# Optimization experiments

Measured on AMD Instinct MI355X. Metric: run time of the kernel, lower is better.

Reference implementation:

```python
import jax, jax.numpy as jnp
import numpy as np

B, N, D, H, ND = 16, 512, 768, 12, 32
DK = D // H  # 64
GRID = 11    # hard-coded 11x11 patch grid in SpatialCirclePosition.patch


def setup_inputs() -> dict:
    key = jax.random.key(0)
    ks = jax.random.split(key, 10)
    features = jax.random.normal(ks[0], (B, N, D), dtype=jnp.float32)
    boxes = jax.random.uniform(ks[1], (B, N, 4), dtype=jnp.float32)  # normalized [0,1]
    sizes_wh = jax.random.randint(ks[2], (B, 2), 512, 1024).astype(jnp.int32)
    image_sizes = jnp.concatenate([sizes_wh, sizes_wh], axis=-1)  # (B,4) = [w,h,w,h]
    s = 0.02
    Wq = jax.random.normal(ks[3], (D, D), dtype=jnp.float32) * s
    Wk = jax.random.normal(ks[4], (D, D), dtype=jnp.float32) * s
    Wv = jax.random.normal(ks[5], (D, D), dtype=jnp.float32) * s
    Wo = jax.random.normal(ks[6], (D, D), dtype=jnp.float32) * s
    bq = jnp.zeros((D,), jnp.float32); bk = jnp.zeros((D,), jnp.float32)
    bv = jnp.zeros((D,), jnp.float32); bo = jnp.zeros((D,), jnp.float32)
    gamma = jnp.ones((D,), jnp.float32); beta = jnp.zeros((D,), jnp.float32)
    dist_emb = jax.random.normal(ks[7], (ND, H), dtype=jnp.float32) * s
    return {"features": features, "boxes": boxes, "image_sizes": image_sizes,
            "Wq": Wq, "bq": bq, "Wk": Wk, "bk": bk, "Wv": Wv, "bv": bv,
            "Wo": Wo, "bo": bo, "gamma": gamma, "beta": beta, "dist_emb": dist_emb}


def _patch_bins(boxes_norm, image_sizes):
    # boxes_norm: (B,N,4) in [0,1]; image_sizes: (B,4)=[w,h,w,h] int
    sizes_f = image_sizes.astype(jnp.float32)
    boxes = boxes_norm * sizes_f[:, None, :]                       # pixel boxes
    spa = jnp.floor_divide(sizes_f[:, :2], 11.0)                   # (B,2) size_per_area
    lb = jnp.arange(GRID, dtype=jnp.float32)                       # (11,)
    hb = lb + 1.0
    wlb = lb[None, :] * spa[:, 0:1]; whb = hb[None, :] * spa[:, 0:1]   # (B,11)
    hlb = lb[None, :] * spa[:, 1:2]; hhb = hb[None, :] * spa[:, 1:2]
    cx = jnp.floor_divide(boxes[..., 0] + boxes[..., 2], 2.0)      # (B,N)
    cy = jnp.floor_divide(boxes[..., 1] + boxes[..., 3], 2.0)
    mx = (wlb[:, None, :] <= cx[..., None]) & (cx[..., None] <= whb[:, None, :])  # (B,N,11)
    my = (hlb[:, None, :] <= cy[..., None]) & (cy[..., None] <= hhb[:, None, :])
    px = jnp.argmax(mx.astype(jnp.float32), axis=-1)               # (B,N) int
    py = jnp.argmax(my.astype(jnp.float32), axis=-1)
    return px.astype(jnp.float32), py.astype(jnp.float32)


def _dist_bins(boxes_norm, image_sizes):
    px, py = _patch_bins(boxes_norm, image_sizes)
    dx = px[:, None, :] - px[:, :, None]                           # (B,N,N)
    dy = py[:, None, :] - py[:, :, None]
    dist = jnp.sqrt(dx * dx + dy * dy) * 2.0
    return dist.astype(jnp.int32)                                  # truncation == .long()


def reference(features, boxes, image_sizes, Wq, bq, Wk, bk, Wv, bv, Wo, bo, gamma, beta, dist_emb):
    # LayerNorm(d_model), eps matches torch default 1e-5
    mu = jnp.mean(features, axis=-1, keepdims=True)
    var = jnp.mean(jnp.square(features - mu), axis=-1, keepdims=True)
    x = (features - mu) * jax.lax.rsqrt(var + 1e-5) * gamma + beta

    bins = _dist_bins(boxes, image_sizes)                          # (B,N,N) int32
    dist_bias = dist_emb[bins]                                     # (B,N,N,H)
    dist_bias = jnp.transpose(dist_bias, (0, 3, 1, 2))             # (B,H,N,N)

    bsz, nq, _ = x.shape
    q = (x @ Wq.T + bq).reshape(bsz, nq, H, DK).transpose(0, 2, 1, 3)  # (B,H,N,DK)
    k = (x @ Wk.T + bk).reshape(bsz, nq, H, DK).transpose(0, 2, 1, 3)
    v = (x @ Wv.T + bv).reshape(bsz, nq, H, DK).transpose(0, 2, 1, 3)

    att = jnp.einsum('bhqd,bhkd->bhqk', q, k) / np.sqrt(DK).astype(np.float32)
    att = jax.nn.softmax(att + dist_bias, axis=-1)                 # (B,H,N,N)
    out = jnp.einsum('bhqk,bhkd->bhqd', att, v)
    out = out.transpose(0, 2, 1, 3).reshape(bsz, nq, H * DK)
    out = out @ Wo.T + bo
    return out, att
```

## Files before the change

### kernel.cpp

```cpp
#include <hip/hip_runtime.h>
#include <hip/hip_bf16.h>

typedef unsigned char uchar;
typedef __attribute__((ext_vector_type(8))) short bf16x8;
typedef __attribute__((ext_vector_type(4))) float f32x4;

__device__ __forceinline__ unsigned short f2bf(float f) {
  union { float f; unsigned int u; } v; v.f = f;
  unsigned int u = v.u + 0x7fffu + ((v.u >> 16) & 1u);
  return (unsigned short)(u >> 16);
}

__device__ __forceinline__ void async_cp16(void* lds, const void* g) {
  __builtin_amdgcn_global_load_lds(
      (const __attribute__((address_space(1))) unsigned int*)g,
      (__attribute__((address_space(3))) unsigned int*)lds, 16, 0, 0);
}

__global__ void pxpy_kernel(const float* __restrict__ boxes, const int* __restrict__ isz,
                            unsigned short* __restrict__ ppk) {
  int idx = blockIdx.x * 256 + threadIdx.x;
  int b = idx >> 9;
  float w = (float)isz[b * 4 + 0];
  float h = (float)isz[b * 4 + 1];
  float b0 = boxes[idx * 4 + 0] * w;
  float b1 = boxes[idx * 4 + 1] * h;
  float b2 = boxes[idx * 4 + 2] * w;
  float b3 = boxes[idx * 4 + 3] * h;
  float spw = floorf(w / 11.0f);
  float sph = floorf(h / 11.0f);
  float cx = floorf((b0 + b2) * 0.5f);
  float cy = floorf((b1 + b3) * 0.5f);
  int pxi = 0, pyi = 0;
  bool fx = false, fy = false;
  for (int j = 0; j < 11; ++j) {
    float jf = (float)j;
    if (!fx && jf * spw <= cx && cx <= (jf + 1.0f) * spw) { pxi = j; fx = true; }
    if (!fy && jf * sph <= cy && cy <= (jf + 1.0f) * sph) { pyi = j; fy = true; }
  }
  ppk[idx] = (unsigned short)(pxi | (pyi << 8));
}

__global__ __launch_bounds__(256) void ln_kernel(const float* __restrict__ f,
                                                 const float* __restrict__ gamma,
                                                 const float* __restrict__ beta,
                                                 unsigned short* __restrict__ x) {
  const int r = blockIdx.x;
  const int t = threadIdx.x;
  const float* row = f + (size_t)r * 768;
  float e0 = row[t], e1 = row[t + 256], e2 = row[t + 512];
  float s = e0 + e1 + e2;
#pragma unroll
  for (int off = 32; off > 0; off >>= 1) s += __shfl_down(s, off);
  __shared__ float red[4];
  const int wid = t >> 6;
  if ((t & 63) == 0) red[wid] = s;
  __syncthreads();
  float mean = (red[0] + red[1] + red[2] + red[3]) * (1.0f / 768.0f);
  __syncthreads();
  float d0 = e0 - mean, d1 = e1 - mean, d2 = e2 - mean;
  float v = d0 * d0 + d1 * d1 + d2 * d2;
#pragma unroll
  for (int off = 32; off > 0; off >>= 1) v += __shfl_down(v, off);
  if ((t & 63) == 0) red[wid] = v;
  __syncthreads();
  float var = (red[0] + red[1] + red[2] + red[3]) * (1.0f / 768.0f);
  float rs = rsqrtf(var + 1e-5f);
  x[(size_t)r * 768 + t]       = f2bf(d0 * rs * gamma[t] + beta[t]);
  x[(size_t)r * 768 + t + 256] = f2bf(d1 * rs * gamma[t + 256] + beta[t + 256]);
  x[(size_t)r * 768 + t + 512] = f2bf(d2 * rs * gamma[t + 512] + beta[t + 512]);
}

__global__ void wprep_kernel(const float* __restrict__ Wq, const float* __restrict__ Wk,
                             const float* __restrict__ Wv, const float* __restrict__ Wo,
                             const float* __restrict__ bq, const float* __restrict__ bk,
                             const float* __restrict__ bv,
                             unsigned short* __restrict__ wcat, unsigned short* __restrict__ wo,
                             float* __restrict__ bcat) {
  int idx = blockIdx.x * 256 + threadIdx.x;
  if (idx < 1769472) {
    int n = idx / 768, k = idx % 768;
    float v = (n < 768) ? Wq[n * 768 + k]
            : (n < 1536) ? Wk[(n - 768) * 768 + k]
                         : Wv[(n - 1536) * 768 + k];
    wcat[idx] = f2bf(v);
  } else {
    int j = idx - 1769472;
    wo[j] = f2bf(Wo[j]);
  }
  if (idx < 2304)
    bcat[idx] = (idx < 768) ? bq[idx] : (idx < 1536) ? bk[idx - 768] : bv[idx - 1536];
}

template <bool OUTF32>
__global__ __launch_bounds__(256) void gemm_bt(const unsigned short* __restrict__ A,
                                               const unsigned short* __restrict__ Bt,
                                               const float* __restrict__ bias,
                                               void* __restrict__ Cout, int K, int ldc) {
  __shared__ unsigned short a_lds[2][128 * 32];
  __shared__ unsigned short b_lds[2][128 * 32];
  const int m0 = blockIdx.x * 128, n0 = blockIdx.y * 128;
  const int tid = threadIdx.x;
  const int lane = tid & 63, wid = tid >> 6;
  const int ln = lane & 15, quad = lane >> 4;
  const int wm = (wid & 1) * 64, wn = (wid >> 1) * 64;
  f32x4 acc[16] = {};
  const int nk = K >> 5;
#pragma unroll
  for (int rep = 0; rep < 2; ++rep) {
    int c = rep * 256 + tid;
    int row = c >> 2, e0 = (c & 3) << 3;
    async_cp16(&a_lds[0][c * 8], A + (size_t)(m0 + row) * K + e0);
    async_cp16(&b_lds[0][c * 8], Bt + (size_t)(n0 + row) * K + e0);
  }
  __syncthreads();
  for (int kc = 0; kc < nk; ++kc) {
    const int cur = kc & 1;
    if (kc + 1 < nk) {
      const int k0 = (kc + 1) << 5;
#pragma unroll
      for (int rep = 0; rep < 2; ++rep) {
        int c = rep * 256 + tid;
        int row = c >> 2, e0 = (c & 3) << 3;
        async_cp16(&a_lds[cur ^ 1][c * 8], A + (size_t)(m0 + row) * K + k0 + e0);
        async_cp16(&b_lds[cur ^ 1][c * 8], Bt + (size_t)(n0 + row) * K + k0 + e0);
      }
    }
    bf16x8 af[4], bfr[4];
#pragma unroll
    for (int i = 0; i < 4; ++i)
      af[i] = *(const bf16x8*)&a_lds[cur][(wm + i * 16 + ln) * 32 + quad * 8];
#pragma unroll
    for (int j = 0; j < 4; ++j)
      bfr[j] = *(const bf16x8*)&b_lds[cur][(wn + j * 16 + ln) * 32 + quad * 8];
#pragma unroll
    for (int i = 0; i < 4; ++i)
#pragma unroll
      for (int j = 0; j < 4; ++j)
        acc[i * 4 + j] = __builtin_amdgcn_mfma_f32_16x16x32_bf16(af[i], bfr[j], acc[i * 4 + j], 0, 0, 0);
    __syncthreads();
  }
#pragma unroll
  for (int i = 0; i < 4; ++i)
#pragma unroll
    for (int j = 0; j < 4; ++j)
#pragma unroll
      for (int r = 0; r < 4; ++r) {
        int rr = m0 + wm + i * 16 + quad * 4 + r;
        int cc = n0 + wn + j * 16 + ln;
        float v = acc[i * 4 + j][r] + bias[cc];
        if (OUTF32) ((float*)Cout)[(size_t)rr * ldc + cc] = v;
        else ((unsigned short*)Cout)[(size_t)rr * ldc + cc] = f2bf(v);
      }
}

__global__ __launch_bounds__(256) void attn_fused(const unsigned short* __restrict__ qkv,
                                                  const unsigned short* __restrict__ ppk,
                                                  const float* __restrict__ dist_emb,
                                                  float* __restrict__ att,
                                                  unsigned short* __restrict__ attnout) {
  const int bidx = blockIdx.x;
  const int qt = bidx & 7;
  const int h = (bidx >> 3) % 12;
  const int b = bidx / 96;
  __shared__ unsigned short qs[64 * 72];
  __shared__ unsigned short ks[2][64 * 72];
  __shared__ float lut[448];
  __shared__ unsigned short pklds[512];
  const int tid = threadIdx.x;
  const int lane = tid & 63, wid = tid >> 6;
  const int ln = lane & 15, quad = lane >> 4;
  for (int t = tid; t < 441; t += 256) {
    int dx = t / 21 - 10, dy = t % 21 - 10;
    int bin = (int)(sqrtf((float)(dx * dx + dy * dy)) * 2.0f);
    lut[t] = dist_emb[bin * 12 + h];
  }
  if (tid < 64)
    *(uint4*)&pklds[tid * 8] = *(const uint4*)(ppk + (size_t)b * 512 + tid * 8);

  {
    int i0 = tid >> 3, e0 = (tid & 7) * 8;
    *(uint4*)&qs[i0 * 72 + e0] =
        *(const uint4*)(qkv + (size_t)(b * 512 + qt * 64 + i0) * 2304 + h * 64 + e0);
    *(uint4*)&qs[(i0 + 32) * 72 + e0] =
        *(const uint4*)(qkv + (size_t)(b * 512 + qt * 64 + i0 + 32) * 2304 + h * 64 + e0);
  }
  const int si = tid >> 3, se = (tid & 7) * 8;
  const unsigned short* kbase = qkv + (size_t)(b * 512) * 2304 + 768 + h * 64 + se;
  const unsigned short* vbase = qkv + (size_t)(b * 512) * 2304 + 1536 + h * 64 + se;
  uint4 kr0 = *(const uint4*)(kbase + (size_t)si * 2304);
  uint4 kr1 = *(const uint4*)(kbase + (size_t)(si + 32) * 2304);
  __syncthreads();
  bf16x8 a0 = *(const bf16x8*)&qs[(wid * 16 + ln) * 72 + quad * 8];
  bf16x8 a1 = *(const bf16x8*)&qs[(wid * 16 + ln) * 72 + 32 + quad * 8];
  *(uint4*)&ks[0][si * 72 + se] = kr0;
  *(uint4*)&ks[0][(si + 32) * 72 + se] = kr1;
  __syncthreads();
  f32x4 acc[32] = {};
  for (int kc = 0; kc < 8; ++kc) {
    const unsigned short* cur = ks[kc & 1];
    if (kc < 7) {
      kr0 = *(const uint4*)(kbase + (size_t)((kc + 1) * 64 + si) * 2304);
      kr1 = *(const uint4*)(kbase + (size_t)((kc + 1) * 64 + si + 32) * 2304);
    }
    __builtin_amdgcn_s_setprio(1);
#pragma unroll
    for (int t = 0; t < 4; ++t) {
      bf16x8 b0 = *(const bf16x8*)&cur[(t * 16 + ln) * 72 + quad * 8];
      bf16x8 b1 = *(const bf16x8*)&cur[(t * 16 + ln) * 72 + 32 + quad * 8];
      acc[kc * 4 + t] = __builtin_amdgcn_mfma_f32_16x16x32_bf16(a0, b0, acc[kc * 4 + t], 0, 0, 0);
      acc[kc * 4 + t] = __builtin_amdgcn_mfma_f32_16x16x32_bf16(a1, b1, acc[kc * 4 + t], 0, 0, 0);
    }
    __builtin_amdgcn_s_setprio(0);
    if (kc < 7) {
      unsigned short* nxt = ks[(kc + 1) & 1];
      *(uint4*)&nxt[si * 72 + se] = kr0;
      *(uint4*)&nxt[(si + 32) * 72 + se] = kr1;
      __syncthreads();
    }
  }
  uint4 vr0 = *(const uint4*)(vbase + (size_t)si * 2304);
  uint4 vr1 = *(const uint4*)(vbase + (size_t)(si + 32) * 2304);

  const int brow0 = qt * 64 + wid * 16 + quad * 4;
  int cr[4];
#pragma unroll
  for (int r = 0; r < 4; ++r) {
    int pq = pklds[brow0 + r];
    cr[r] = 220 - (pq & 255) * 21 - (pq >> 8);
  }
#pragma unroll
  for (int i = 0; i < 32; ++i) {
    int col = (i >> 2) * 64 + (i & 3) * 16 + ln;
    int pk = pklds[col];
    int base = (pk & 255) * 21 + (pk >> 8);
#pragma unroll
    for (int r = 0; r < 4; ++r) {
      acc[i][r] = acc[i][r] * 0.125f + lut[base + cr[r]];
    }
  }
  float inv[4];
#pragma unroll
  for (int r = 0; r < 4; ++r) {
    float m = -1e30f;
#pragma unroll
    for (int i = 0; i < 32; ++i) m = fmaxf(m, acc[i][r]);
    m = fmaxf(m, __shfl_xor(m, 1));
    m = fmaxf(m, __shfl_xor(m, 2));
    m = fmaxf(m, __shfl_xor(m, 4));
    m = fmaxf(m, __shfl_xor(m, 8));
    float s = 0.f;
#pragma unroll
    for (int i = 0; i < 32; ++i) { float p = __expf(acc[i][r] - m); acc[i][r] = p; s += p; }
    s += __shfl_xor(s, 1); s += __shfl_xor(s, 2); s += __shfl_xor(s, 4); s += __shfl_xor(s, 8);
    inv[r] = 1.0f / s;
  }
#pragma unroll
  for (int i = 0; i < 32; ++i)
#pragma unroll
    for (int r = 0; r < 4; ++r) acc[i][r] *= inv[r];

  {
    const unsigned short* xs = (const unsigned short*)&vr0;
#pragma unroll
    for (int j = 0; j < 8; ++j) {
      int d = se + j;
      ks[0][d * 72 + (si ^ (((d >> 3) & 7) << 3))] = xs[j];
    }
    xs = (const unsigned short*)&vr1;
#pragma unroll
    for (int j = 0; j < 8; ++j) {
      int d = se + j;
      ks[0][d * 72 + ((si + 32) ^ (((d >> 3) & 7) << 3))] = xs[j];
    }
  }
  __syncthreads();
  f32x4 acc_o[4] = {};
  float* ob = att + (size_t)((b * 12 + h) * 512) * 512;
  for (int kc = 0; kc < 8; ++kc) {
    const unsigned short* cur = ks[kc & 1];
    if (kc < 7) {
      vr0 = *(const uint4*)(vbase + (size_t)((kc + 1) * 64 + si) * 2304);
      vr1 = *(const uint4*)(vbase + (size_t)((kc + 1) * 64 + si + 32) * 2304);
    }
#pragma unroll
    for (int t = 0; t < 4; ++t)
#pragma unroll
      for (int r = 0; r < 4; ++r) {
        int row = wid * 16 + quad * 4 + r;
        int col = (t * 16 + ln) ^ (((row >> 2) & 7) << 3);
        qs[row * 72 + col] = f2bf(acc[kc * 4 + t][r]);
      }
    __builtin_amdgcn_s_setprio(1);
#pragma unroll
    for (int kk = 0; kk < 2; ++kk) {
      int prow = wid * 16 + ln;
      int pcol = (kk * 32 + quad * 8) ^ (((prow >> 2) & 7) << 3);
      bf16x8 af = *(const bf16x8*)&qs[prow * 72 + pcol];
#pragma unroll
      for (int ct = 0; ct < 4; ++ct) {
        int d = ct * 16 + ln;
        int vcol = (kk * 32 + quad * 8) ^ (((d >> 3) & 7) << 3);
        bf16x8 bg = *(const bf16x8*)&cur[d * 72 + vcol];
        acc_o[ct] = __builtin_amdgcn_mfma_f32_16x16x32_bf16(af, bg, acc_o[ct], 0, 0, 0);
      }
    }
    __builtin_amdgcn_s_setprio(0);
#pragma unroll
    for (int t = 0; t < 4; ++t)
#pragma unroll
      for (int r = 0; r < 4; ++r)
        ob[(size_t)(brow0 + r) * 512 + kc * 64 + t * 16 + ln] = acc[kc * 4 + t][r];
    if (kc < 7) {
      unsigned short* nxt = ks[(kc + 1) & 1];
      const unsigned short* xs = (const unsigned short*)&vr0;
#pragma unroll
      for (int j = 0; j < 8; ++j) {
        int d = se + j;
        nxt[d * 72 + (si ^ (((d >> 3) & 7) << 3))] = xs[j];
      }
      xs = (const unsigned short*)&vr1;
#pragma unroll
      for (int j = 0; j < 8; ++j) {
        int d = se + j;
        nxt[d * 72 + ((si + 32) ^ (((d >> 3) & 7) << 3))] = xs[j];
      }
      __syncthreads();
    }
  }
#pragma unroll
  for (int ct = 0; ct < 4; ++ct)
#pragma unroll
    for (int r = 0; r < 4; ++r) {
      int m = b * 512 + qt * 64 + wid * 16 + quad * 4 + r;
      int cc = h * 64 + ct * 16 + ln;
      attnout[(size_t)m * 768 + cc] = f2bf(acc_o[ct][r]);
    }
}

extern "C" void kernel_launch(void* const* d_in, const int* in_sizes, int n_in,
                              void* d_out, int out_size, void* d_ws, size_t ws_size,
                              hipStream_t stream) {
  const float* features = (const float*)d_in[0];
  const float* boxes    = (const float*)d_in[1];
  const int*   isz      = (const int*)d_in[2];
  const float* Wq = (const float*)d_in[3];
  const float* bq = (const float*)d_in[4];
  const float* Wk = (const float*)d_in[5];
  const float* bk = (const float*)d_in[6];
  const float* Wv = (const float*)d_in[7];
  const float* bv = (const float*)d_in[8];
  const float* Wo = (const float*)d_in[9];
  const float* bo = (const float*)d_in[10];
  const float* gamma = (const float*)d_in[11];
  const float* beta  = (const float*)d_in[12];
  const float* dist_emb = (const float*)d_in[13];

  float* out = (float*)d_out;
  float* att = out + (size_t)8192 * 768;

  char* w = (char*)d_ws;
  unsigned short* ppk = (unsigned short*)w;     w += 8192 * 2;
  unsigned short* x = (unsigned short*)w;       w += (size_t)8192 * 768 * 2;
  unsigned short* wcat = (unsigned short*)w;    w += (size_t)2304 * 768 * 2;
  unsigned short* wo = (unsigned short*)w;      w += (size_t)768 * 768 * 2;
  float* bcat = (float*)w;                      w += 2304 * 4;
  unsigned short* qkv = (unsigned short*)w;     w += (size_t)8192 * 2304 * 2;
  unsigned short* attnout = (unsigned short*)w; w += (size_t)8192 * 768 * 2;

  pxpy_kernel<<<32, 256, 0, stream>>>(boxes, isz, ppk);
  ln_kernel<<<8192, 256, 0, stream>>>(features, gamma, beta, x);
  wprep_kernel<<<9216, 256, 0, stream>>>(Wq, Wk, Wv, Wo, bq, bk, bv, wcat, wo, bcat);
  gemm_bt<false><<<dim3(64, 18), 256, 0, stream>>>(x, wcat, bcat, qkv, 768, 2304);
  attn_fused<<<1536, 256, 0, stream>>>(qkv, ppk, dist_emb, att, attnout);
  gemm_bt<true><<<dim3(64, 6), 256, 0, stream>>>(attnout, wo, bo, out, 768, 768);
}
```

Before: 397.7 us.

## Triple-buffer K/V tiles with two-ahead prefetch and swizzle block order for XCD locality

The attention kernel now keeps three LDS buffers for K/V tiles and register-prefetches two tiles ahead, so global loads have more time to land. It also drops one barrier per iteration and overlaps the first V-tile load with the tail of the QK loop. Block indices in both the GEMM and attention kernels are remapped so that neighbouring work lands on the same XCD, which should improve L2 reuse. The cost is more registers and LDS per block, which may lower occupancy given the large accumulator array. The GEMM swizzle also hard-codes a grid width of 64.

```diff
diff --git a/kernel.cpp b/kernel.cpp
--- a/kernel.cpp
+++ b/kernel.cpp
@@ -99,7 +99,10 @@
                                                void* __restrict__ Cout, int K, int ldc) {
   __shared__ unsigned short a_lds[2][128 * 32];
   __shared__ unsigned short b_lds[2][128 * 32];
-  const int m0 = blockIdx.x * 128, n0 = blockIdx.y * 128;
+  const int lin = blockIdx.x + blockIdx.y * 64;
+  const int cpx = (gridDim.x * gridDim.y) >> 3;
+  const int swz = (lin & 7) * cpx + (lin >> 3);
+  const int m0 = (swz & 63) * 128, n0 = (swz >> 6) * 128;
   const int tid = threadIdx.x;
   const int lane = tid & 63, wid = tid >> 6;
   const int ln = lane & 15, quad = lane >> 4;
@@ -159,17 +162,24 @@
                                                   const float* __restrict__ dist_emb,
                                                   float* __restrict__ att,
                                                   unsigned short* __restrict__ attnout) {
-  const int bidx = blockIdx.x;
+  const int bidx = (blockIdx.x & 7) * 192 + (blockIdx.x >> 3);
   const int qt = bidx & 7;
   const int h = (bidx >> 3) % 12;
   const int b = bidx / 96;
   __shared__ unsigned short qs[64 * 72];
-  __shared__ unsigned short ks[2][64 * 72];
+  __shared__ unsigned short ks[3][64 * 72];
   __shared__ float lut[448];
   __shared__ unsigned short pklds[512];
   const int tid = threadIdx.x;
   const int lane = tid & 63, wid = tid >> 6;
   const int ln = lane & 15, quad = lane >> 4;
+  const int si = tid >> 3, se = (tid & 7) * 8;
+  const unsigned short* kbase = qkv + (size_t)(b * 512) * 2304 + 768 + h * 64 + se;
+  const unsigned short* vbase = qkv + (size_t)(b * 512) * 2304 + 1536 + h * 64 + se;
+  uint4 pA0 = *(const uint4*)(kbase + (size_t)si * 2304);
+  uint4 pA1 = *(const uint4*)(kbase + (size_t)(si + 32) * 2304);
+  uint4 pB0 = *(const uint4*)(kbase + (size_t)(64 + si) * 2304);
+  uint4 pB1 = *(const uint4*)(kbase + (size_t)(64 + si + 32) * 2304);
   for (int t = tid; t < 441; t += 256) {
     int dx = t / 21 - 10, dy = t % 21 - 10;
     int bin = (int)(sqrtf((float)(dx * dx + dy * dy)) * 2.0f);
@@ -177,7 +187,6 @@
   }
   if (tid < 64)
     *(uint4*)&pklds[tid * 8] = *(const uint4*)(ppk + (size_t)b * 512 + tid * 8);
-
   {
     int i0 = tid >> 3, e0 = (tid & 7) * 8;
     *(uint4*)&qs[i0 * 72 + e0] =
@@ -185,42 +194,64 @@
     *(uint4*)&qs[(i0 + 32) * 72 + e0] =
         *(const uint4*)(qkv + (size_t)(b * 512 + qt * 64 + i0 + 32) * 2304 + h * 64 + e0);
   }
-  const int si = tid >> 3, se = (tid & 7) * 8;
-  const unsigned short* kbase = qkv + (size_t)(b * 512) * 2304 + 768 + h * 64 + se;
-  const unsigned short* vbase = qkv + (size_t)(b * 512) * 2304 + 1536 + h * 64 + se;
-  uint4 kr0 = *(const uint4*)(kbase + (size_t)si * 2304);
-  uint4 kr1 = *(const uint4*)(kbase + (size_t)(si + 32) * 2304);
+  *(uint4*)&ks[0][si * 72 + se] = pA0;
+  *(uint4*)&ks[0][(si + 32) * 72 + se] = pA1;
   __syncthreads();
   bf16x8 a0 = *(const bf16x8*)&qs[(wid * 16 + ln) * 72 + quad * 8];
   bf16x8 a1 = *(const bf16x8*)&qs[(wid * 16 + ln) * 72 + 32 + quad * 8];
-  *(uint4*)&ks[0][si * 72 + se] = kr0;
-  *(uint4*)&ks[0][(si + 32) * 72 + se] = kr1;
-  __syncthreads();
   f32x4 acc[32] = {};
-  for (int kc = 0; kc < 8; ++kc) {
-    const unsigned short* cur = ks[kc & 1];
-    if (kc < 7) {
-      kr0 = *(const uint4*)(kbase + (size_t)((kc + 1) * 64 + si) * 2304);
-      kr1 = *(const uint4*)(kbase + (size_t)((kc + 1) * 64 + si + 32) * 2304);
-    }
-    __builtin_amdgcn_s_setprio(1);
-#pragma unroll
-    for (int t = 0; t < 4; ++t) {
-      bf16x8 b0 = *(const bf16x8*)&cur[(t * 16 + ln) * 72 + quad * 8];
-      bf16x8 b1 = *(const bf16x8*)&cur[(t * 16 + ln) * 72 + 32 + quad * 8];
-      acc[kc * 4 + t] = __builtin_amdgcn_mfma_f32_16x16x32_bf16(a0, b0, acc[kc * 4 + t], 0, 0, 0);
-      acc[kc * 4 + t] = __builtin_amdgcn_mfma_f32_16x16x32_bf16(a1, b1, acc[kc * 4 + t], 0, 0, 0);
-    }
-    __builtin_amdgcn_s_setprio(0);
-    if (kc < 7) {
-      unsigned short* nxt = ks[(kc + 1) & 1];
-      *(uint4*)&nxt[si * 72 + se] = kr0;
-      *(uint4*)&nxt[(si + 32) * 72 + se] = kr1;
+#pragma unroll
+  for (int c = 0; c < 8; c += 2) {
+    {
+      if (c + 2 < 8) {
+        pA0 = *(const uint4*)(kbase + (size_t)((c + 2) * 64 + si) * 2304);
+        pA1 = *(const uint4*)(kbase + (size_t)((c + 2) * 64 + si + 32) * 2304);
+      } else {
+        pA0 = *(const uint4*)(vbase + (size_t)si * 2304);
+        pA1 = *(const uint4*)(vbase + (size_t)(si + 32) * 2304);
+      }
+      unsigned short* nb = ks[(c + 1) % 3];
+      *(uint4*)&nb[si * 72 + se] = pB0;
+      *(uint4*)&nb[(si + 32) * 72 + se] = pB1;
+      const unsigned short* cur = ks[c % 3];
+      __builtin_amdgcn_s_setprio(1);
+#pragma unroll
+      for (int t = 0; t < 4; ++t) {
+        bf16x8 b0 = *(const bf16x8*)&cur[(t * 16 + ln) * 72 + quad * 8];
+        bf16x8 b1 = *(const bf16x8*)&cur[(t * 16 + ln) * 72 + 32 + quad * 8];
+        acc[c * 4 + t] = __builtin_amdgcn_mfma_f32_16x16x32_bf16(a0, b0, acc[c * 4 + t], 0, 0, 0);
+        acc[c * 4 + t] = __builtin_amdgcn_mfma_f32_16x16x32_bf16(a1, b1, acc[c * 4 + t], 0, 0, 0);
+      }
+      __builtin_amdgcn_s_setprio(0);
       __syncthreads();
     }
-  }
-  uint4 vr0 = *(const uint4*)(vbase + (size_t)si * 2304);
-  uint4 vr1 = *(const uint4*)(vbase + (size_t)(si + 32) * 2304);
+    {
+      const int c1 = c + 1;
+      if (c1 + 2 < 8) {
+        pB0 = *(const uint4*)(kbase + (size_t)((c1 + 2) * 64 + si) * 2304);
+        pB1 = *(const uint4*)(kbase + (size_t)((c1 + 2) * 64 + si + 32) * 2304);
+      } else {
+        pB0 = *(const uint4*)(vbase + (size_t)(64 + si) * 2304);
+        pB1 = *(const uint4*)(vbase + (size_t)(64 + si + 32) * 2304);
+      }
+      if (c1 < 7) {
+        unsigned short* nb = ks[(c1 + 1) % 3];
+        *(uint4*)&nb[si * 72 + se] = pA0;
+        *(uint4*)&nb[(si + 32) * 72 + se] = pA1;
+      }
+      const unsigned short* cur = ks[c1 % 3];
+      __builtin_amdgcn_s_setprio(1);
+#pragma unroll
+      for (int t = 0; t < 4; ++t) {
+        bf16x8 b0 = *(const bf16x8*)&cur[(t * 16 + ln) * 72 + quad * 8];
+        bf16x8 b1 = *(const bf16x8*)&cur[(t * 16 + ln) * 72 + 32 + quad * 8];
+        acc[c1 * 4 + t] = __builtin_amdgcn_mfma_f32_16x16x32_bf16(a0, b0, acc[c1 * 4 + t], 0, 0, 0);
+        acc[c1 * 4 + t] = __builtin_amdgcn_mfma_f32_16x16x32_bf16(a1, b1, acc[c1 * 4 + t], 0, 0, 0);
+      }
+      __builtin_amdgcn_s_setprio(0);
+      __syncthreads();
+    }
+  }
 
   const int brow0 = qt * 64 + wid * 16 + quad * 4;
   int cr[4];
@@ -261,13 +292,13 @@
     for (int r = 0; r < 4; ++r) acc[i][r] *= inv[r];
 
   {
-    const unsigned short* xs = (const unsigned short*)&vr0;
+    const unsigned short* xs = (const unsigned short*)&pA0;
 #pragma unroll
     for (int j = 0; j < 8; ++j) {
       int d = se + j;
       ks[0][d * 72 + (si ^ (((d >> 3) & 7) << 3))] = xs[j];
     }
-    xs = (const unsigned short*)&vr1;
+    xs = (const unsigned short*)&pA1;
 #pragma unroll
     for (int j = 0; j < 8; ++j) {
       int d = se + j;
@@ -277,55 +308,108 @@
   __syncthreads();
   f32x4 acc_o[4] = {};
   float* ob = att + (size_t)((b * 12 + h) * 512) * 512;
-  for (int kc = 0; kc < 8; ++kc) {
-    const unsigned short* cur = ks[kc & 1];
-    if (kc < 7) {
-      vr0 = *(const uint4*)(vbase + (size_t)((kc + 1) * 64 + si) * 2304);
-      vr1 = *(const uint4*)(vbase + (size_t)((kc + 1) * 64 + si + 32) * 2304);
-    }
-#pragma unroll
-    for (int t = 0; t < 4; ++t)
-#pragma unroll
-      for (int r = 0; r < 4; ++r) {
-        int row = wid * 16 + quad * 4 + r;
-        int col = (t * 16 + ln) ^ (((row >> 2) & 7) << 3);
-        qs[row * 72 + col] = f2bf(acc[kc * 4 + t][r]);
-      }
-    __builtin_amdgcn_s_setprio(1);
-#pragma unroll
-    for (int kk = 0; kk < 2; ++kk) {
-      int prow = wid * 16 + ln;
-      int pcol = (kk * 32 + quad * 8) ^ (((prow >> 2) & 7) << 3);
-      bf16x8 af = *(const bf16x8*)&qs[prow * 72 + pcol];
-#pragma unroll
-      for (int ct = 0; ct < 4; ++ct) {
-        int d = ct * 16 + ln;
-        int vcol = (kk * 32 + quad * 8) ^ (((d >> 3) & 7) << 3);
-        bf16x8 bg = *(const bf16x8*)&cur[d * 72 + vcol];
-        acc_o[ct] = __builtin_amdgcn_mfma_f32_16x16x32_bf16(af, bg, acc_o[ct], 0, 0, 0);
-      }
-    }
-    __builtin_amdgcn_s_setprio(0);
-#pragma unroll
-    for (int t = 0; t < 4; ++t)
-#pragma unroll
-      for (int r = 0; r < 4; ++r)
-        ob[(size_t)(brow0 + r) * 512 + kc * 64 + t * 16 + ln] = acc[kc * 4 + t][r];
-    if (kc < 7) {
-      unsigned short* nxt = ks[(kc + 1) & 1];
-      const unsigned short* xs = (const unsigned short*)&vr0;
+#pragma unroll
+  for (int pc = 0; pc < 8; pc += 2) {
+    {
+      if (pc + 2 < 8) {
+        pA0 = *(const uint4*)(vbase + (size_t)((pc + 2) * 64 + si) * 2304);
+        pA1 = *(const uint4*)(vbase + (size_t)((pc + 2) * 64 + si + 32) * 2304);
+      }
+      unsigned short* nb = ks[(pc + 1) % 3];
+      const unsigned short* xs = (const unsigned short*)&pB0;
 #pragma unroll
       for (int j = 0; j < 8; ++j) {
         int d = se + j;
-        nxt[d * 72 + (si ^ (((d >> 3) & 7) << 3))] = xs[j];
-      }
-      xs = (const unsigned short*)&vr1;
+        nb[d * 72 + (si ^ (((d >> 3) & 7) << 3))] = xs[j];
+      }
+      xs = (const unsigned short*)&pB1;
 #pragma unroll
       for (int j = 0; j < 8; ++j) {
         int d = se + j;
-        nxt[d * 72 + ((si + 32) ^ (((d >> 3) & 7) << 3))] = xs[j];
-      }
+        nb[d * 72 + ((si + 32) ^ (((d >> 3) & 7) << 3))] = xs[j];
+      }
+#pragma unroll
+      for (int t = 0; t < 4; ++t)
+#pragma unroll
+        for (int r = 0; r < 4; ++r) {
+          int row = wid * 16 + quad * 4 + r;
+          int col = (t * 16 + ln) ^ (((row >> 2) & 7) << 3);
+          qs[row * 72 + col] = f2bf(acc[pc * 4 + t][r]);
+        }
+      const unsigned short* cur = ks[pc % 3];
+      __builtin_amdgcn_s_setprio(1);
+#pragma unroll
+      for (int kk = 0; kk < 2; ++kk) {
+        int prow = wid * 16 + ln;
+        int pcol = (kk * 32 + quad * 8) ^ (((prow >> 2) & 7) << 3);
+        bf16x8 af = *(const bf16x8*)&qs[prow * 72 + pcol];
+#pragma unroll
+        for (int ct = 0; ct < 4; ++ct) {
+          int d = ct * 16 + ln;
+          int vcol = (kk * 32 + quad * 8) ^ (((d >> 3) & 7) << 3);
+          bf16x8 bg = *(const bf16x8*)&cur[d * 72 + vcol];
+          acc_o[ct] = __builtin_amdgcn_mfma_f32_16x16x32_bf16(af, bg, acc_o[ct], 0, 0, 0);
+        }
+      }
+      __builtin_amdgcn_s_setprio(0);
+#pragma unroll
+      for (int t = 0; t < 4; ++t)
+#pragma unroll
+        for (int r = 0; r < 4; ++r)
+          ob[(size_t)(brow0 + r) * 512 + pc * 64 + t * 16 + ln] = acc[pc * 4 + t][r];
       __syncthreads();
+    }
+    {
+      const int p1 = pc + 1;
+      if (p1 + 2 < 8) {
+        pB0 = *(const uint4*)(vbase + (size_t)((p1 + 2) * 64 + si) * 2304);
+        pB1 = *(const uint4*)(vbase + (size_t)((p1 + 2) * 64 + si + 32) * 2304);
+      }
+      if (p1 < 7) {
+        unsigned short* nb = ks[(p1 + 1) % 3];
+        const unsigned short* xs = (const unsigned short*)&pA0;
+#pragma unroll
+        for (int j = 0; j < 8; ++j) {
+          int d = se + j;
+          nb[d * 72 + (si ^ (((d >> 3) & 7) << 3))] = xs[j];
+        }
+        xs = (const unsigned short*)&pA1;
+#pragma unroll
+        for (int j = 0; j < 8; ++j) {
+          int d = se + j;
+          nb[d * 72 + ((si + 32) ^ (((d >> 3) & 7) << 3))] = xs[j];
+        }
+      }
+#pragma unroll
+      for (int t = 0; t < 4; ++t)
+#pragma unroll
+        for (int r = 0; r < 4; ++r) {
+          int row = wid * 16 + quad * 4 + r;
+          int col = (t * 16 + ln) ^ (((row >> 2) & 7) << 3);
+          qs[row * 72 + col] = f2bf(acc[p1 * 4 + t][r]);
+        }
+      const unsigned short* cur = ks[p1 % 3];
+      __builtin_amdgcn_s_setprio(1);
+#pragma unroll
+      for (int kk = 0; kk < 2; ++kk) {
+        int prow = wid * 16 + ln;
+        int pcol = (kk * 32 + quad * 8) ^ (((prow >> 2) & 7) << 3);
+        bf16x8 af = *(const bf16x8*)&qs[prow * 72 + pcol];
+#pragma unroll
+        for (int ct = 0; ct < 4; ++ct) {
+          int d = ct * 16 + ln;
+          int vcol = (kk * 32 + quad * 8) ^ (((d >> 3) & 7) << 3);
+          bf16x8 bg = *(const bf16x8*)&cur[d * 72 + vcol];
+          acc_o[ct] = __builtin_amdgcn_mfma_f32_16x16x32_bf16(af, bg, acc_o[ct], 0, 0, 0);
+        }
+      }
+      __builtin_amdgcn_s_setprio(0);
+#pragma unroll
+      for (int t = 0; t < 4; ++t)
+#pragma unroll
+        for (int r = 0; r < 4; ++r)
+          ob[(size_t)(brow0 + r) * 512 + p1 * 64 + t * 16 + ln] = acc[p1 * 4 + t][r];
+      if (p1 < 7) __syncthreads();
     }
   }
 #pragma unroll
```

New measurement: 405.5 us. Within noise of the previous version (+2.0%).

## Load Q/K tiles via async global-to-LDS copies with XOR swizzle, hoist att stores

Applied to the files above, without the earlier changes.

Q and K tiles are now copied straight from global memory into LDS with global_load_lds. The swizzle is applied to the global source address, so the LDS rows become unpadded 64-element rows. The K double-buffer prefetch is issued at the top of each iteration, which removes the register staging and the separate LDS store step. The attention probabilities are written to global memory in one pass before the P·V loop and pre-packed to bf16 pairs, instead of being converted and stored inside that loop. The risks are higher register pressure from the fully unrolled loops and the extra packed arrays, and reliance on barriers waiting for the async LDS copies to land.

```diff
diff --git a/kernel.cpp b/kernel.cpp
--- a/kernel.cpp
+++ b/kernel.cpp
@@ -170,6 +170,21 @@
   const int tid = threadIdx.x;
   const int lane = tid & 63, wid = tid >> 6;
   const int ln = lane & 15, quad = lane >> 4;
+
+  const int c0 = tid, c1 = 256 + tid;
+  const int r0 = c0 >> 3, g0 = c0 & 7;
+  const int r1 = c1 >> 3, g1 = c1 & 7;
+  const int sc0 = (g0 ^ (r0 & 7)) * 8;
+  const int sc1 = (g1 ^ (r1 & 7)) * 8;
+  const unsigned short* qg0 = qkv + (size_t)(b * 512 + qt * 64 + r0) * 2304 + h * 64 + sc0;
+  const unsigned short* qg1 = qkv + (size_t)(b * 512 + qt * 64 + r1) * 2304 + h * 64 + sc1;
+  const unsigned short* kg0 = qkv + (size_t)(b * 512 + r0) * 2304 + 768 + h * 64 + sc0;
+  const unsigned short* kg1 = qkv + (size_t)(b * 512 + r1) * 2304 + 768 + h * 64 + sc1;
+  async_cp16(&qs[c0 * 8], qg0);
+  async_cp16(&qs[c1 * 8], qg1);
+  async_cp16(&ks[0][c0 * 8], kg0);
+  async_cp16(&ks[0][c1 * 8], kg1);
+
   for (int t = tid; t < 441; t += 256) {
     int dx = t / 21 - 10, dy = t % 21 - 10;
     int bin = (int)(sqrtf((float)(dx * dx + dy * dy)) * 2.0f);
@@ -177,48 +192,37 @@
   }
   if (tid < 64)
     *(uint4*)&pklds[tid * 8] = *(const uint4*)(ppk + (size_t)b * 512 + tid * 8);
-
-  {
-    int i0 = tid >> 3, e0 = (tid & 7) * 8;
-    *(uint4*)&qs[i0 * 72 + e0] =
-        *(const uint4*)(qkv + (size_t)(b * 512 + qt * 64 + i0) * 2304 + h * 64 + e0);
-    *(uint4*)&qs[(i0 + 32) * 72 + e0] =
-        *(const uint4*)(qkv + (size_t)(b * 512 + qt * 64 + i0 + 32) * 2304 + h * 64 + e0);
-  }
-  const int si = tid >> 3, se = (tid & 7) * 8;
-  const unsigned short* kbase = qkv + (size_t)(b * 512) * 2304 + 768 + h * 64 + se;
-  const unsigned short* vbase = qkv + (size_t)(b * 512) * 2304 + 1536 + h * 64 + se;
-  uint4 kr0 = *(const uint4*)(kbase + (size_t)si * 2304);
-  uint4 kr1 = *(const uint4*)(kbase + (size_t)(si + 32) * 2304);
-  __syncthreads();
-  bf16x8 a0 = *(const bf16x8*)&qs[(wid * 16 + ln) * 72 + quad * 8];
-  bf16x8 a1 = *(const bf16x8*)&qs[(wid * 16 + ln) * 72 + 32 + quad * 8];
-  *(uint4*)&ks[0][si * 72 + se] = kr0;
-  *(uint4*)&ks[0][(si + 32) * 72 + se] = kr1;
-  __syncthreads();
+  __syncthreads();
+
+  const int arow = wid * 16 + ln;
+  const int rs8 = (ln & 7);
+  bf16x8 a0 = *(const bf16x8*)&qs[arow * 64 + ((quad ^ rs8) * 8)];
+  bf16x8 a1 = *(const bf16x8*)&qs[arow * 64 + (((quad + 4) ^ rs8) * 8)];
+
   f32x4 acc[32] = {};
+  const size_t kstep = (size_t)64 * 2304;
+#pragma unroll
   for (int kc = 0; kc < 8; ++kc) {
+    if (kc < 7) {
+      async_cp16(&ks[(kc + 1) & 1][c0 * 8], kg0 + (size_t)(kc + 1) * kstep);
+      async_cp16(&ks[(kc + 1) & 1][c1 * 8], kg1 + (size_t)(kc + 1) * kstep);
+    }
     const unsigned short* cur = ks[kc & 1];
-    if (kc < 7) {
-      kr0 = *(const uint4*)(kbase + (size_t)((kc + 1) * 64 + si) * 2304);
-      kr1 = *(const uint4*)(kbase + (size_t)((kc + 1) * 64 + si + 32) * 2304);
-    }
     __builtin_amdgcn_s_setprio(1);
 #pragma unroll
     for (int t = 0; t < 4; ++t) {
-      bf16x8 b0 = *(const bf16x8*)&cur[(t * 16 + ln) * 72 + quad * 8];
-      bf16x8 b1 = *(const bf16x8*)&cur[(t * 16 + ln) * 72 + 32 + quad * 8];
+      const int brow = t * 16 + ln;
+      bf16x8 b0 = *(const bf16x8*)&cur[brow * 64 + ((quad ^ rs8) * 8)];
+      bf16x8 b1 = *(const bf16x8*)&cur[brow * 64 + (((quad + 4) ^ rs8) * 8)];
       acc[kc * 4 + t] = __builtin_amdgcn_mfma_f32_16x16x32_bf16(a0, b0, acc[kc * 4 + t], 0, 0, 0);
       acc[kc * 4 + t] = __builtin_amdgcn_mfma_f32_16x16x32_bf16(a1, b1, acc[kc * 4 + t], 0, 0, 0);
     }
     __builtin_amdgcn_s_setprio(0);
-    if (kc < 7) {
-      unsigned short* nxt = ks[(kc + 1) & 1];
-      *(uint4*)&nxt[si * 72 + se] = kr0;
-      *(uint4*)&nxt[(si + 32) * 72 + se] = kr1;
-      __syncthreads();
-    }
-  }
+    if (kc < 7) __syncthreads();
+  }
+
+  const int si = tid >> 3, se = (tid & 7) * 8;
+  const unsigned short* vbase = qkv + (size_t)(b * 512) * 2304 + 1536 + h * 64 + se;
   uint4 vr0 = *(const uint4*)(vbase + (size_t)si * 2304);
   uint4 vr1 = *(const uint4*)(vbase + (size_t)(si + 32) * 2304);
 
@@ -260,6 +264,21 @@
 #pragma unroll
     for (int r = 0; r < 4; ++r) acc[i][r] *= inv[r];
 
+  float* ob = att + (size_t)((b * 12 + h) * 512) * 512;
+#pragma unroll
+  for (int i = 0; i < 32; ++i) {
+    int col = (i >> 2) * 64 + (i & 3) * 16 + ln;
+#pragma unroll
+    for (int r = 0; r < 4; ++r)
+      ob[(size_t)(brow0 + r) * 512 + col] = acc[i][r];
+  }
+  unsigned int p01[32], p23[32];
+#pragma unroll
+  for (int i = 0; i < 32; ++i) {
+    p01[i] = (unsigned int)f2bf(acc[i][0]) | ((unsigned int)f2bf(acc[i][1]) << 16);
+    p23[i] = (unsigned int)f2bf(acc[i][2]) | ((unsigned int)f2bf(acc[i][3]) << 16);
+  }
+
   {
     const unsigned short* xs = (const unsigned short*)&vr0;
 #pragma unroll
@@ -276,7 +295,9 @@
   }
   __syncthreads();
   f32x4 acc_o[4] = {};
-  float* ob = att + (size_t)((b * 12 + h) * 512) * 512;
+  const int prow0 = wid * 16 + quad * 4;
+  const int psw = ((wid * 4 + quad) & 7) << 3;
+#pragma unroll
   for (int kc = 0; kc < 8; ++kc) {
     const unsigned short* cur = ks[kc & 1];
     if (kc < 7) {
@@ -284,13 +305,15 @@
       vr1 = *(const uint4*)(vbase + (size_t)((kc + 1) * 64 + si + 32) * 2304);
     }
 #pragma unroll
-    for (int t = 0; t < 4; ++t)
-#pragma unroll
-      for (int r = 0; r < 4; ++r) {
-        int row = wid * 16 + quad * 4 + r;
-        int col = (t * 16 + ln) ^ (((row >> 2) & 7) << 3);
-        qs[row * 72 + col] = f2bf(acc[kc * 4 + t][r]);
-      }
+    for (int t = 0; t < 4; ++t) {
+      int col = (t * 16 + ln) ^ psw;
+      unsigned int a01 = p01[kc * 4 + t];
+      unsigned int a23 = p23[kc * 4 + t];
+      qs[(prow0 + 0) * 72 + col] = (unsigned short)a01;
+      qs[(prow0 + 1) * 72 + col] = (unsigned short)(a01 >> 16);
+      qs[(prow0 + 2) * 72 + col] = (unsigned short)a23;
+      qs[(prow0 + 3) * 72 + col] = (unsigned short)(a23 >> 16);
+    }
     __builtin_amdgcn_s_setprio(1);
 #pragma unroll
     for (int kk = 0; kk < 2; ++kk) {
@@ -306,11 +329,6 @@
       }
     }
     __builtin_amdgcn_s_setprio(0);
-#pragma unroll
-    for (int t = 0; t < 4; ++t)
-#pragma unroll
-      for (int r = 0; r < 4; ++r)
-        ob[(size_t)(brow0 + r) * 512 + kc * 64 + t * 16 + ln] = acc[kc * 4 + t][r];
     if (kc < 7) {
       unsigned short* nxt = ks[(kc + 1) & 1];
       const unsigned short* xs = (const unsigned short*)&vr0;
```

Measured after the change: 408.9 us. +2.8%, slower.
